# Kernel tuning notes

Hardware: AMD Instinct MI355X
Metric: run time of the kernel (lower is better)

## Reference

```python
import jax, jax.numpy as jnp
import numpy as np

N = 100000   # nodes
E = 1600000  # edges
G = 64       # graphs in batch
F_IN = 128
H = 128
SV = 64
AD = 32


def setup_inputs() -> dict:
    key = jax.random.key(0)
    ks = jax.random.split(key, 12)
    s = 0.05
    return {
        "x": jax.random.normal(ks[0], (N, F_IN), jnp.float32),
        "edge_index": jax.random.randint(ks[1], (2, E), 0, N, dtype=jnp.int64),
        "batch": jnp.sort(jax.random.randint(ks[2], (N,), 0, G, dtype=jnp.int64)),
        "state_vector": jax.random.normal(ks[3], (G, SV), jnp.float32),
        "action": jax.random.normal(ks[4], (G, AD), jnp.float32),
        "W1": jax.random.normal(ks[5], (F_IN, H), jnp.float32) * s,
        "b1": jnp.zeros((H,), jnp.float32),
        "W2": jax.random.normal(ks[6], (H, H), jnp.float32) * s,
        "b2": jnp.zeros((H,), jnp.float32),
        "Wf1": jax.random.normal(ks[7], (H + SV + AD, 256), jnp.float32) * s,
        "bf1": jnp.zeros((256,), jnp.float32),
        "Wf2": jax.random.normal(ks[8], (256, 256), jnp.float32) * s,
        "bf2": jnp.zeros((256,), jnp.float32),
        "Wo": jax.random.normal(ks[9], (256, 1), jnp.float32) * s,
        "bo": jnp.zeros((1,), jnp.float32),
    }


def gcn_conv(x, W, b, src, dst, deg_inv_sqrt):
    # PyG GCNConv: h = x @ W; aggregate D^-1/2 (A+I) D^-1/2 h; + b
    h = x @ W
    norm = deg_inv_sqrt[src] * deg_inv_sqrt[dst]          # [E]
    agg = jax.ops.segment_sum(h[src] * norm[:, None], dst, num_segments=N)
    agg = agg + h * (deg_inv_sqrt * deg_inv_sqrt)[:, None]  # self loops
    return agg + b


def reference(x, edge_index, batch, state_vector, action,
              W1, b1, W2, b2, Wf1, bf1, Wf2, bf2, Wo, bo):
    src, dst = edge_index[0], edge_index[1]
    # degree after adding self loops (aggregation index = dst, PyG default flow)
    deg = jax.ops.segment_sum(jnp.ones((E,), jnp.float32), dst, num_segments=N) + 1.0
    deg_inv_sqrt = jax.lax.rsqrt(deg)

    h = jax.nn.relu(gcn_conv(x, W1, b1, src, dst, deg_inv_sqrt))
    h = jax.nn.relu(gcn_conv(h, W2, b2, src, dst, deg_inv_sqrt))

    # global_mean_pool over graph ids
    sums = jax.ops.segment_sum(h, batch, num_segments=G)
    cnts = jax.ops.segment_sum(jnp.ones((N,), jnp.float32), batch, num_segments=G)
    pooled = sums / jnp.maximum(cnts, 1.0)[:, None]       # [G, H]

    z = jnp.concatenate([pooled, state_vector, action], axis=1)  # [G, H+SV+AD]
    z = jax.nn.relu(z @ Wf1 + bf1)
    z = jax.nn.relu(z @ Wf2 + bf2)
    return z @ Wo + bo                                     # [G, 1]
```

## Files before the change

kernel.cpp:

```cpp
#include <hip/hip_runtime.h>
#include <hip/hip_bf16.h>
#include <stdint.h>

#define N_NODES 100000
#define N_EDGES 1600000
#define N_GRAPHS 64
#define HDIM 128

#define BUCKET_SHIFT 9
#define NBUCK ((N_NODES + 511) >> 9)
#define CAP 9728
#define SCAT_CHUNK 8192
#define SCAT_NBLK ((N_EDGES + SCAT_CHUNK - 1) / SCAT_CHUNK)
#define GB_NBLK ((N_NODES + 255) / 256)

typedef __bf16 bf16x8 __attribute__((ext_vector_type(8)));
typedef float f32x4 __attribute__((ext_vector_type(4)));
typedef float f32x2 __attribute__((ext_vector_type(2)));

__global__ __launch_bounds__(256) void setup_kernel(const int* __restrict__ batch,
                                                    int* __restrict__ gstart,
                                                    const float* __restrict__ W1,
                                                    const float* __restrict__ W2,
                                                    __hip_bfloat16* __restrict__ Wt1,
                                                    __hip_bfloat16* __restrict__ Wt2,
                                                    int* __restrict__ gcur,
                                                    float* __restrict__ psum) {
    int bid = blockIdx.x;
    if (bid < GB_NBLK) {
        int i = bid * 256 + threadIdx.x;
        if (i >= N_NODES) return;
        int b = batch[i];
        int prev = (i == 0) ? -1 : batch[i - 1];
        for (int g = prev + 1; g <= b; ++g) gstart[g] = i;
        if (i == N_NODES - 1) {
            for (int g = b + 1; g <= N_GRAPHS; ++g) gstart[g] = N_NODES;
        }
    } else if (bid < GB_NBLK + 128) {
        int t = bid - GB_NBLK;
        const float* W = (t < 64) ? W1 : W2;
        __hip_bfloat16* Wt = (t < 64) ? Wt1 : Wt2;
        int bb = t & 63;
        int n = bb * 2 + (threadIdx.x >> 7);
        int k = threadIdx.x & 127;
        Wt[n * 128 + k] = __float2bfloat16(W[k * 128 + n]);
    } else {
        int i = (bid - GB_NBLK - 128) * 256 + threadIdx.x;
        if (i < NBUCK) gcur[i] = i * CAP;
        int j = i - NBUCK;
        if (j >= 0 && j < N_GRAPHS * HDIM) psum[j] = 0.f;
    }
}
#define SETUP_NBLK (GB_NBLK + 128 + (NBUCK + N_GRAPHS * HDIM + 255) / 256)

__global__ __launch_bounds__(256) void scatter_kernel(const int* __restrict__ src,
                                                      const int* __restrict__ dst,
                                                      int* __restrict__ gcur,
                                                      int* __restrict__ sorted, int E) {
    __shared__ int hist[NBUCK];
    __shared__ int base_s[NBUCK];
    int tid = threadIdx.x;
    int e0 = blockIdx.x * SCAT_CHUNK;
    int sv[SCAT_CHUNK / 256], dv[SCAT_CHUNK / 256];
#pragma unroll
    for (int j = 0; j < SCAT_CHUNK / 256; j++) {
        int e = e0 + (j << 8) + tid;
        if (e < E) { sv[j] = src[e]; dv[j] = dst[e]; } else { sv[j] = -1; dv[j] = -1; }
    }
    if (tid < NBUCK) hist[tid] = 0;
    __syncthreads();
#pragma unroll
    for (int j = 0; j < SCAT_CHUNK / 256; j++)
        if (dv[j] >= 0) atomicAdd(&hist[dv[j] >> BUCKET_SHIFT], 1);
    __syncthreads();
    if (tid < NBUCK) {
        int c = hist[tid];
        base_s[tid] = (c > 0) ? atomicAdd(&gcur[tid], c) : 0;
    }
    __syncthreads();
    if (tid < NBUCK) hist[tid] = 0;
    __syncthreads();
#pragma unroll
    for (int j = 0; j < SCAT_CHUNK / 256; j++) {
        if (dv[j] >= 0) {
            int b = dv[j] >> BUCKET_SHIFT;
            int idx = atomicAdd(&hist[b], 1);
            sorted[base_s[b] + idx] = ((dv[j] & 511) << 17) | sv[j];
        }
    }
}

__global__ __launch_bounds__(256) void bucket_build_kernel(const int* __restrict__ sorted,
                                                           const int* __restrict__ gcur,
                                                           int2* __restrict__ rs2,
                                                           float* __restrict__ dis,
                                                           int* __restrict__ csr_src) {
    __shared__ int edges[CAP];
    __shared__ int cnt[512];
    __shared__ int excl[512];
    __shared__ int ps[256];
    int b = blockIdx.x, tid = threadIdx.x;
    cnt[tid] = 0; cnt[tid + 256] = 0;
    int node0 = b << BUCKET_SHIFT;
    int lo = b * CAP, hi = gcur[b];
    int ne = hi - lo;
    for (int i = tid; i < ne; i += 256) edges[i] = sorted[lo + i];
    __syncthreads();
    for (int i = tid; i < ne; i += 256)
        atomicAdd(&cnt[((unsigned)edges[i]) >> 17], 1);
    __syncthreads();
    int c0 = cnt[2 * tid], c1 = cnt[2 * tid + 1];
    ps[tid] = c0 + c1;
    __syncthreads();
#pragma unroll
    for (int off = 1; off < 256; off <<= 1) {
        int t = (tid >= off) ? ps[tid - off] : 0;
        __syncthreads();
        ps[tid] += t;
        __syncthreads();
    }
    int pex = ps[tid] - (c0 + c1);
    excl[2 * tid] = pex;
    excl[2 * tid + 1] = pex + c0;
    __syncthreads();
#pragma unroll
    for (int k = 0; k < 2; k++) {
        int li = tid + k * 256;
        int node = node0 + li;
        if (node < N_NODES) {
            int st = lo + excl[li] + li;
            int c = cnt[li];
            rs2[node] = make_int2(st, st + c + 1);
            dis[node] = rsqrtf((float)c + 1.0f);
            csr_src[st + c] = node;
        }
    }
    cnt[tid] = 0; cnt[tid + 256] = 0;
    __syncthreads();
    for (int i = tid; i < ne; i += 256) {
        int v = edges[i];
        int li = ((unsigned)v) >> 17;
        int idx = atomicAdd(&cnt[li], 1);
        csr_src[lo + excl[li] + li + idx] = v & 0x1FFFF;
    }
}

template<bool A_FP32>
__global__ __launch_bounds__(256) void gemm_mfma_kernel(const void* __restrict__ Av,
                                                        const __hip_bfloat16* __restrict__ Wt,
                                                        const float* __restrict__ scale,
                                                        unsigned char* __restrict__ C, int nrows) {
    __shared__ float Cs[64 * 132];
    int tid = threadIdx.x;
    int wave = tid >> 6, lane = tid & 63;
    int quad = lane >> 4, l16 = lane & 15;
    int row0 = blockIdx.x * 64;
    int arow = row0 + wave * 16 + l16;
    int arow_c = min(arow, nrows - 1);

    const __hip_bfloat16* A16 = (const __hip_bfloat16*)Av;
    const float* A32 = (const float*)Av;

    f32x4 acc[8];
#pragma unroll
    for (int t = 0; t < 8; t++) acc[t] = (f32x4){0.f, 0.f, 0.f, 0.f};

#pragma unroll
    for (int kt = 0; kt < 4; kt++) {
        int kbase = kt * 32 + quad * 8;
        union { bf16x8 v; __hip_bfloat16 h[8]; uint4 u; } au;
        if (A_FP32) {
            const float* ap = A32 + (size_t)arow_c * 128 + kbase;
            float4 u0 = *(const float4*)ap;
            float4 u1 = *(const float4*)(ap + 4);
            au.h[0] = __float2bfloat16(u0.x); au.h[1] = __float2bfloat16(u0.y);
            au.h[2] = __float2bfloat16(u0.z); au.h[3] = __float2bfloat16(u0.w);
            au.h[4] = __float2bfloat16(u1.x); au.h[5] = __float2bfloat16(u1.y);
            au.h[6] = __float2bfloat16(u1.z); au.h[7] = __float2bfloat16(u1.w);
        } else {
            au.u = *(const uint4*)(A16 + (size_t)arow_c * 128 + kbase);
        }
#pragma unroll
        for (int t = 0; t < 8; t++) {
            bf16x8 b = *(const bf16x8*)(Wt + (size_t)(t * 16 + l16) * 128 + kbase);
            acc[t] = __builtin_amdgcn_mfma_f32_16x16x32_bf16(au.v, b, acc[t], 0, 0, 0);
        }
    }

    int rbase = wave * 16 + quad * 4;
    float s[4];
#pragma unroll
    for (int r = 0; r < 4; r++) s[r] = scale[min(row0 + rbase + r, nrows - 1)];
#pragma unroll
    for (int t = 0; t < 8; t++) {
#pragma unroll
        for (int r = 0; r < 4; r++)
            Cs[(rbase + r) * 132 + t * 16 + l16] = acc[t][r] * s[r];
    }
    __syncthreads();

#pragma unroll
    for (int p = 0; p < 4; p++) {
        int g = p * 256 + tid;
        int row = g >> 4, c8 = (g & 15) * 8;
        int grow = row0 + row;
        if (grow < nrows) {
            const float* cp = &Cs[row * 132 + c8];
            float4 v0 = *(const float4*)cp;
            float4 v1 = *(const float4*)(cp + 4);
            int w0 = __builtin_amdgcn_cvt_pk_fp8_f32(v0.x, v0.y, 0, false);
            w0 = __builtin_amdgcn_cvt_pk_fp8_f32(v0.z, v0.w, w0, true);
            int w1 = __builtin_amdgcn_cvt_pk_fp8_f32(v1.x, v1.y, 0, false);
            w1 = __builtin_amdgcn_cvt_pk_fp8_f32(v1.z, v1.w, w1, true);
            *(uint2*)(C + (size_t)grow * 128 + c8) = make_uint2((unsigned)w0, (unsigned)w1);
        }
    }
}

__device__ __forceinline__ void accum8p(f32x2* acc, uint2 u) {
    acc[0] += __builtin_amdgcn_cvt_pk_f32_fp8((int)u.x, false);
    acc[1] += __builtin_amdgcn_cvt_pk_f32_fp8((int)u.x, true);
    acc[2] += __builtin_amdgcn_cvt_pk_f32_fp8((int)u.y, false);
    acc[3] += __builtin_amdgcn_cvt_pk_f32_fp8((int)u.y, true);
}

__global__ __launch_bounds__(256, 8) void agg_kernel(const unsigned char* __restrict__ h8,
                                                     const float* __restrict__ dis,
                                                     const int2* __restrict__ rs2,
                                                     const int* __restrict__ csr_src,
                                                     const float* __restrict__ bias,
                                                     __hip_bfloat16* __restrict__ out, int n) {
    int wid = threadIdx.x >> 6;
    int lane = threadIdx.x & 63;
    int half = lane >> 5;
    int q = lane >> 4;
    int f = lane & 15;
    int l32 = lane & 31;
    int sub = q & 1;
    int hb = half << 5;
    unsigned fo = (unsigned)(f * 8);

    int nodeA = blockIdx.x * 8 + wid * 2;
    if (nodeA >= n) return;
    int nodeB = nodeA + 1;
    bool hasB = nodeB < n;
    int myNode = half ? (hasB ? nodeB : nodeA) : nodeA;

    int2 se = rs2[myNode];
    int i0 = se.x;
    int deg = se.y - se.x;
    if (half && !hasB) deg = 0;
    float dn = dis[myNode];

    f32x2 acc[4];
#pragma unroll
    for (int j = 0; j < 4; j++) acc[j] = (f32x2){0.f, 0.f};

    for (int base = 0; base < deg; base += 32) {
        int cnt = min(deg - base, 32);
        int idx = csr_src[i0 + base + min(l32, cnt - 1)];
        int e = 0;
        for (; e + 16 <= cnt; e += 16) {
            int s0 = __shfl(idx, hb + e + sub, 64);
            int s1 = __shfl(idx, hb + e + 2 + sub, 64);
            int s2 = __shfl(idx, hb + e + 4 + sub, 64);
            int s3 = __shfl(idx, hb + e + 6 + sub, 64);
            int s4 = __shfl(idx, hb + e + 8 + sub, 64);
            int s5 = __shfl(idx, hb + e + 10 + sub, 64);
            int s6 = __shfl(idx, hb + e + 12 + sub, 64);
            int s7 = __shfl(idx, hb + e + 14 + sub, 64);
            uint2 u0 = *(const uint2*)(h8 + (unsigned)(s0 << 7) + fo);
            uint2 u1 = *(const uint2*)(h8 + (unsigned)(s1 << 7) + fo);
            uint2 u2 = *(const uint2*)(h8 + (unsigned)(s2 << 7) + fo);
            uint2 u3 = *(const uint2*)(h8 + (unsigned)(s3 << 7) + fo);
            uint2 u4 = *(const uint2*)(h8 + (unsigned)(s4 << 7) + fo);
            uint2 u5 = *(const uint2*)(h8 + (unsigned)(s5 << 7) + fo);
            uint2 u6 = *(const uint2*)(h8 + (unsigned)(s6 << 7) + fo);
            uint2 u7 = *(const uint2*)(h8 + (unsigned)(s7 << 7) + fo);
            accum8p(acc, u0);
            accum8p(acc, u1);
            accum8p(acc, u2);
            accum8p(acc, u3);
            accum8p(acc, u4);
            accum8p(acc, u5);
            accum8p(acc, u6);
            accum8p(acc, u7);
        }
        if (e < cnt) {
            int r = cnt - 1;
#pragma unroll
            for (int k = 0; k < 8; k++) {
                int ln = e + 2 * k + sub;
                int s = __shfl(idx, hb + min(ln, r), 64);
                uint2 u = *(const uint2*)(h8 + (unsigned)(s << 7) + fo);
                if (ln > r) { u.x = 0u; u.y = 0u; }
                accum8p(acc, u);
            }
        }
    }

#pragma unroll
    for (int j = 0; j < 4; j++) {
        f32x2 v = acc[j];
        v[0] += __shfl_down(v[0], 16, 64);
        v[1] += __shfl_down(v[1], 16, 64);
        acc[j] = v;
    }

    if (sub == 0 && (half == 0 || hasB)) {
        float4 b0 = *(const float4*)(bias + f * 8);
        float4 b1 = *(const float4*)(bias + f * 8 + 4);
        float r0 = fmaxf(fmaf(acc[0][0], dn, b0.x), 0.f);
        float r1 = fmaxf(fmaf(acc[0][1], dn, b0.y), 0.f);
        float r2 = fmaxf(fmaf(acc[1][0], dn, b0.z), 0.f);
        float r3 = fmaxf(fmaf(acc[1][1], dn, b0.w), 0.f);
        float r4 = fmaxf(fmaf(acc[2][0], dn, b1.x), 0.f);
        float r5 = fmaxf(fmaf(acc[2][1], dn, b1.y), 0.f);
        float r6 = fmaxf(fmaf(acc[3][0], dn, b1.z), 0.f);
        float r7 = fmaxf(fmaf(acc[3][1], dn, b1.w), 0.f);
        __hip_bfloat162 p0 = __float22bfloat162_rn(make_float2(r0, r1));
        __hip_bfloat162 p1 = __float22bfloat162_rn(make_float2(r2, r3));
        __hip_bfloat162 p2 = __float22bfloat162_rn(make_float2(r4, r5));
        __hip_bfloat162 p3 = __float22bfloat162_rn(make_float2(r6, r7));
        uint4 pk;
        pk.x = *(unsigned int*)&p0; pk.y = *(unsigned int*)&p1;
        pk.z = *(unsigned int*)&p2; pk.w = *(unsigned int*)&p3;
        *(uint4*)(out + (size_t)myNode * 128 + f * 8) = pk;
    }
}

#define POOL_ROWS 128
__global__ __launch_bounds__(256) void pool_kernel(const __hip_bfloat16* __restrict__ h,
                                                   const int* __restrict__ batch,
                                                   const int* __restrict__ gstart,
                                                   float* __restrict__ psum, int n) {
    __shared__ float red[16 * 128];
    int tid = threadIdx.x;
    int rr = tid >> 4, fg = tid & 15;
    int r0 = blockIdx.x * POOL_ROWS;
    if (r0 >= n) return;
    int r1 = min(n, r0 + POOL_ROWS);
    int g = batch[r0];
    int seg_lo = r0;
    while (seg_lo < r1) {
        while (gstart[g + 1] <= seg_lo) g++;
        int seg_hi = min(r1, gstart[g + 1]);
        float a[8];
#pragma unroll
        for (int j = 0; j < 8; j++) a[j] = 0.f;
        for (int r = seg_lo + rr; r < seg_hi; r += 16) {
            uint4 u = *(const uint4*)(h + (size_t)r * 128 + fg * 8);
            float2 f0 = __bfloat1622float2(*(__hip_bfloat162*)&u.x);
            float2 f1 = __bfloat1622float2(*(__hip_bfloat162*)&u.y);
            float2 f2 = __bfloat1622float2(*(__hip_bfloat162*)&u.z);
            float2 f3 = __bfloat1622float2(*(__hip_bfloat162*)&u.w);
            a[0] += f0.x; a[1] += f0.y; a[2] += f1.x; a[3] += f1.y;
            a[4] += f2.x; a[5] += f2.y; a[6] += f3.x; a[7] += f3.y;
        }
        *(float4*)&red[rr * 128 + fg * 8] = make_float4(a[0], a[1], a[2], a[3]);
        *(float4*)&red[rr * 128 + fg * 8 + 4] = make_float4(a[4], a[5], a[6], a[7]);
        __syncthreads();
        if (tid < 128) {
            float s = 0.f;
#pragma unroll
            for (int k = 0; k < 16; k++) s += red[k * 128 + tid];
            atomicAdd(&psum[g * 128 + tid], s);
        }
        __syncthreads();
        seg_lo = seg_hi;
    }
}

__global__ __launch_bounds__(256) void mlp_kernel(const float* __restrict__ psum,
                                                  const int* __restrict__ gstart,
                                                  const float* __restrict__ sv,
                                                  const float* __restrict__ act,
                                                  const float* __restrict__ Wf1,
                                                  const float* __restrict__ bf1,
                                                  const float* __restrict__ Wf2,
                                                  const float* __restrict__ bf2,
                                                  const float* __restrict__ Wo,
                                                  const float* __restrict__ bo,
                                                  float* __restrict__ out) {
    int g = blockIdx.x, tid = threadIdx.x;
    __shared__ float z[224];
    __shared__ float z1[256];
    __shared__ float red[256];
    if (tid < 128) {
        int c = gstart[g + 1] - gstart[g];
        float cnt = fmaxf((float)c, 1.f);
        z[tid] = psum[g * 128 + tid] / cnt;
    } else if (tid < 192) {
        z[tid] = sv[g * 64 + (tid - 128)];
    } else if (tid < 224) {
        z[tid] = act[g * 32 + (tid - 192)];
    }
    __syncthreads();
    float a = bf1[tid];
    for (int k = 0; k < 224; k++) a = fmaf(z[k], Wf1[k * 256 + tid], a);
    z1[tid] = fmaxf(a, 0.f);
    __syncthreads();
    float b = bf2[tid];
    for (int k = 0; k < 256; k++) b = fmaf(z1[k], Wf2[k * 256 + tid], b);
    b = fmaxf(b, 0.f);
    red[tid] = b * Wo[tid];
    __syncthreads();
    for (int off = 128; off > 0; off >>= 1) {
        if (tid < off) red[tid] += red[tid + off];
        __syncthreads();
    }
    if (tid == 0) out[g] = red[0] + bo[0];
}

extern "C" void kernel_launch(void* const* d_in, const int* in_sizes, int n_in,
                              void* d_out, int out_size, void* d_ws, size_t ws_size,
                              hipStream_t stream) {
    const float* x   = (const float*)d_in[0];
    const int*   eidx = (const int*)d_in[1];
    const int*   batch = (const int*)d_in[2];
    const float* sv  = (const float*)d_in[3];
    const float* act = (const float*)d_in[4];
    const float* W1  = (const float*)d_in[5];
    const float* b1  = (const float*)d_in[6];
    const float* W2  = (const float*)d_in[7];
    const float* b2  = (const float*)d_in[8];
    const float* Wf1 = (const float*)d_in[9];
    const float* bf1 = (const float*)d_in[10];
    const float* Wf2 = (const float*)d_in[11];
    const float* bf2 = (const float*)d_in[12];
    const float* Wo  = (const float*)d_in[13];
    const float* bo  = (const float*)d_in[14];
    float* out = (float*)d_out;

    const int* srcp = eidx;
    const int* dstp = eidx + N_EDGES;

    char* w = (char*)d_ws;
    int* gcur = (int*)w;               w += (size_t)NBUCK * 4;
    float* psum = (float*)w;           w += (size_t)N_GRAPHS * HDIM * 4;
    int2* rs2 = (int2*)w;              w += (size_t)N_NODES * 8;
    float* dis = (float*)w;            w += (size_t)N_NODES * 4;
    int* gstart = (int*)w;             w += (size_t)(N_GRAPHS + 1) * 4;
    w = (char*)(((uintptr_t)w + 255) & ~(uintptr_t)255);
    int* csr_src = (int*)w;            w += (size_t)NBUCK * CAP * 4;
    w = (char*)(((uintptr_t)w + 255) & ~(uintptr_t)255);
    int* sorted = (int*)w;             w += (size_t)NBUCK * CAP * 4;
    w = (char*)(((uintptr_t)w + 255) & ~(uintptr_t)255);
    __hip_bfloat16* Wt1 = (__hip_bfloat16*)w;   w += (size_t)HDIM * HDIM * 2;
    __hip_bfloat16* Wt2 = (__hip_bfloat16*)w;   w += (size_t)HDIM * HDIM * 2;
    w = (char*)(((uintptr_t)w + 255) & ~(uintptr_t)255);
    unsigned char* hbuf = (unsigned char*)w;    w += (size_t)N_NODES * HDIM;
    w = (char*)(((uintptr_t)w + 255) & ~(uintptr_t)255);
    __hip_bfloat16* abuf = (__hip_bfloat16*)w;  w += (size_t)N_NODES * HDIM * 2;

    setup_kernel<<<SETUP_NBLK, 256, 0, stream>>>(batch, gstart, W1, W2, Wt1, Wt2, gcur, psum);

    scatter_kernel<<<SCAT_NBLK, 256, 0, stream>>>(srcp, dstp, gcur, sorted, N_EDGES);
    bucket_build_kernel<<<NBUCK, 256, 0, stream>>>(sorted, gcur, rs2, dis, csr_src);

    int gemm_blocks = (N_NODES + 63) / 64;
    int agg_blocks = (N_NODES + 7) / 8;

    gemm_mfma_kernel<true><<<gemm_blocks, 256, 0, stream>>>(x, Wt1, dis, hbuf, N_NODES);
    agg_kernel<<<agg_blocks, 256, 0, stream>>>(hbuf, dis, rs2, csr_src, b1, abuf, N_NODES);
    gemm_mfma_kernel<false><<<gemm_blocks, 256, 0, stream>>>(abuf, Wt2, dis, hbuf, N_NODES);
    agg_kernel<<<agg_blocks, 256, 0, stream>>>(hbuf, dis, rs2, csr_src, b2, abuf, N_NODES);

    pool_kernel<<<(N_NODES + POOL_ROWS - 1) / POOL_ROWS, 256, 0, stream>>>(abuf, batch, gstart, psum, N_NODES);
    mlp_kernel<<<N_GRAPHS, 256, 0, stream>>>(psum, gstart, sv, act, Wf1, bf1, Wf2, bf2, Wo, bo, out);
}
```

Measured before the change: 293.9 us.

## Fuse bucket CSR build with first GEMM via global degree counters

Counts node in-degrees with global atomics inside the scatter kernel, so the first GEMM can compute its rsqrt scale directly instead of waiting for the bucket build to produce it. The bucket build and the first GEMM are then merged into one launch with heterogeneous blocks that share a static LDS buffer. This removes one launch and lets the two independent phases overlap. In exchange it adds 1.6M global atomic increments in the scatter kernel, and the merged kernel carries the larger shared-memory footprint, which may lower occupancy for the GEMM blocks.

Result: slower. 348.7 us (+18.6%).

```diff
diff --git a/kernel.cpp b/kernel.cpp
--- a/kernel.cpp
+++ b/kernel.cpp
@@ -12,6 +12,7 @@
 #define CAP 9728
 #define SCAT_CHUNK 8192
 #define SCAT_NBLK ((N_EDGES + SCAT_CHUNK - 1) / SCAT_CHUNK)
+#define GEMM_NBLK ((N_NODES + 63) / 64)
 #define GB_NBLK ((N_NODES + 255) / 256)
 
 typedef __bf16 bf16x8 __attribute__((ext_vector_type(8)));
@@ -25,7 +26,8 @@
                                                     __hip_bfloat16* __restrict__ Wt1,
                                                     __hip_bfloat16* __restrict__ Wt2,
                                                     int* __restrict__ gcur,
-                                                    float* __restrict__ psum) {
+                                                    float* __restrict__ psum,
+                                                    int* __restrict__ deg) {
     int bid = blockIdx.x;
     if (bid < GB_NBLK) {
         int i = bid * 256 + threadIdx.x;
@@ -49,14 +51,17 @@
         if (i < NBUCK) gcur[i] = i * CAP;
         int j = i - NBUCK;
         if (j >= 0 && j < N_GRAPHS * HDIM) psum[j] = 0.f;
-    }
-}
-#define SETUP_NBLK (GB_NBLK + 128 + (NBUCK + N_GRAPHS * HDIM + 255) / 256)
+        int k = j - N_GRAPHS * HDIM;
+        if (k >= 0 && k < N_NODES) deg[k] = 0;
+    }
+}
+#define SETUP_NBLK (GB_NBLK + 128 + (NBUCK + N_GRAPHS * HDIM + N_NODES + 255) / 256)
 
 __global__ __launch_bounds__(256) void scatter_kernel(const int* __restrict__ src,
                                                       const int* __restrict__ dst,
                                                       int* __restrict__ gcur,
-                                                      int* __restrict__ sorted, int E) {
+                                                      int* __restrict__ sorted,
+                                                      int* __restrict__ deg, int E) {
     __shared__ int hist[NBUCK];
     __shared__ int base_s[NBUCK];
     int tid = threadIdx.x;
@@ -71,7 +76,10 @@
     __syncthreads();
 #pragma unroll
     for (int j = 0; j < SCAT_CHUNK / 256; j++)
-        if (dv[j] >= 0) atomicAdd(&hist[dv[j] >> BUCKET_SHIFT], 1);
+        if (dv[j] >= 0) {
+            atomicAdd(&hist[dv[j] >> BUCKET_SHIFT], 1);
+            atomicAdd(&deg[dv[j]], 1);
+        }
     __syncthreads();
     if (tid < NBUCK) {
         int c = hist[tid];
@@ -90,16 +98,16 @@
     }
 }
 
-__global__ __launch_bounds__(256) void bucket_build_kernel(const int* __restrict__ sorted,
-                                                           const int* __restrict__ gcur,
-                                                           int2* __restrict__ rs2,
-                                                           float* __restrict__ dis,
-                                                           int* __restrict__ csr_src) {
-    __shared__ int edges[CAP];
-    __shared__ int cnt[512];
-    __shared__ int excl[512];
-    __shared__ int ps[256];
-    int b = blockIdx.x, tid = threadIdx.x;
+__device__ void bucket_body(const int* __restrict__ sorted,
+                            const int* __restrict__ gcur,
+                            int2* __restrict__ rs2,
+                            float* __restrict__ dis,
+                            int* __restrict__ csr_src, int b, char* smem) {
+    int* edges = (int*)smem;
+    int* cnt = edges + CAP;
+    int* excl = cnt + 512;
+    int* ps = excl + 512;
+    int tid = threadIdx.x;
     cnt[tid] = 0; cnt[tid + 256] = 0;
     int node0 = b << BUCKET_SHIFT;
     int lo = b * CAP, hi = gcur[b];
@@ -145,16 +153,16 @@
     }
 }
 
-template<bool A_FP32>
-__global__ __launch_bounds__(256) void gemm_mfma_kernel(const void* __restrict__ Av,
-                                                        const __hip_bfloat16* __restrict__ Wt,
-                                                        const float* __restrict__ scale,
-                                                        unsigned char* __restrict__ C, int nrows) {
-    __shared__ float Cs[64 * 132];
+template<bool A_FP32, bool DEG_SCALE>
+__device__ void gemm_body(const void* __restrict__ Av,
+                          const __hip_bfloat16* __restrict__ Wt,
+                          const void* __restrict__ scp,
+                          unsigned char* __restrict__ C, int nrows, int bid,
+                          float* Cs ) {
     int tid = threadIdx.x;
     int wave = tid >> 6, lane = tid & 63;
     int quad = lane >> 4, l16 = lane & 15;
-    int row0 = blockIdx.x * 64;
+    int row0 = bid * 64;
     int arow = row0 + wave * 16 + l16;
     int arow_c = min(arow, nrows - 1);
 
@@ -190,7 +198,11 @@
     int rbase = wave * 16 + quad * 4;
     float s[4];
 #pragma unroll
-    for (int r = 0; r < 4; r++) s[r] = scale[min(row0 + rbase + r, nrows - 1)];
+    for (int r = 0; r < 4; r++) {
+        int row = min(row0 + rbase + r, nrows - 1);
+        if (DEG_SCALE) s[r] = rsqrtf((float)((const int*)scp)[row] + 1.0f);
+        else           s[r] = ((const float*)scp)[row];
+    }
 #pragma unroll
     for (int t = 0; t < 8; t++) {
 #pragma unroll
@@ -215,6 +227,31 @@
             *(uint2*)(C + (size_t)grow * 128 + c8) = make_uint2((unsigned)w0, (unsigned)w1);
         }
     }
+}
+
+__global__ __launch_bounds__(256) void build_gemm1_kernel(const int* __restrict__ sorted,
+                                                          const int* __restrict__ gcur,
+                                                          int2* __restrict__ rs2,
+                                                          float* __restrict__ dis,
+                                                          int* __restrict__ csr_src,
+                                                          const float* __restrict__ x,
+                                                          const __hip_bfloat16* __restrict__ Wt1,
+                                                          const int* __restrict__ deg,
+                                                          unsigned char* __restrict__ hbuf) {
+    __shared__ __align__(16) char smem[(CAP + 512 + 512 + 256) * 4];
+    if (blockIdx.x < NBUCK) {
+        bucket_body(sorted, gcur, rs2, dis, csr_src, blockIdx.x, smem);
+    } else {
+        gemm_body<true, true>(x, Wt1, deg, hbuf, N_NODES, blockIdx.x - NBUCK, (float*)smem);
+    }
+}
+
+__global__ __launch_bounds__(256) void gemm_mfma_kernel(const void* __restrict__ Av,
+                                                        const __hip_bfloat16* __restrict__ Wt,
+                                                        const float* __restrict__ scale,
+                                                        unsigned char* __restrict__ C, int nrows) {
+    __shared__ float Cs[64 * 132];
+    gemm_body<false, false>(Av, Wt, scale, C, nrows, blockIdx.x, Cs);
 }
 
 __device__ __forceinline__ void accum8p(f32x2* acc, uint2 u) {
@@ -440,6 +477,7 @@
     float* psum = (float*)w;           w += (size_t)N_GRAPHS * HDIM * 4;
     int2* rs2 = (int2*)w;              w += (size_t)N_NODES * 8;
     float* dis = (float*)w;            w += (size_t)N_NODES * 4;
+    int* deg = (int*)w;                w += (size_t)N_NODES * 4;
     int* gstart = (int*)w;             w += (size_t)(N_GRAPHS + 1) * 4;
     w = (char*)(((uintptr_t)w + 255) & ~(uintptr_t)255);
     int* csr_src = (int*)w;            w += (size_t)NBUCK * CAP * 4;
@@ -453,17 +491,17 @@
     w = (char*)(((uintptr_t)w + 255) & ~(uintptr_t)255);
     __hip_bfloat16* abuf = (__hip_bfloat16*)w;  w += (size_t)N_NODES * HDIM * 2;
 
-    setup_kernel<<<SETUP_NBLK, 256, 0, stream>>>(batch, gstart, W1, W2, Wt1, Wt2, gcur, psum);
-
-    scatter_kernel<<<SCAT_NBLK, 256, 0, stream>>>(srcp, dstp, gcur, sorted, N_EDGES);
-    bucket_build_kernel<<<NBUCK, 256, 0, stream>>>(sorted, gcur, rs2, dis, csr_src);
-
-    int gemm_blocks = (N_NODES + 63) / 64;
+    setup_kernel<<<SETUP_NBLK, 256, 0, stream>>>(batch, gstart, W1, W2, Wt1, Wt2, gcur, psum, deg);
+
+    scatter_kernel<<<SCAT_NBLK, 256, 0, stream>>>(srcp, dstp, gcur, sorted, deg, N_EDGES);
+
+    build_gemm1_kernel<<<NBUCK + GEMM_NBLK, 256, 0, stream>>>(sorted, gcur, rs2, dis, csr_src,
+                                                              x, Wt1, deg, hbuf);
+
     int agg_blocks = (N_NODES + 7) / 8;
 
-    gemm_mfma_kernel<true><<<gemm_blocks, 256, 0, stream>>>(x, Wt1, dis, hbuf, N_NODES);
     agg_kernel<<<agg_blocks, 256, 0, stream>>>(hbuf, dis, rs2, csr_src, b1, abuf, N_NODES);
-    gemm_mfma_kernel<false><<<gemm_blocks, 256, 0, stream>>>(abuf, Wt2, dis, hbuf, N_NODES);
+    gemm_mfma_kernel<<<GEMM_NBLK, 256, 0, stream>>>(abuf, Wt2, dis, hbuf, N_NODES);
     agg_kernel<<<agg_blocks, 256, 0, stream>>>(hbuf, dis, rs2, csr_src, b2, abuf, N_NODES);
 
     pool_kernel<<<(N_NODES + POOL_ROWS - 1) / POOL_ROWS, 256, 0, stream>>>(abuf, batch, gstart, psum, N_NODES);
```

## Fuse global mean-pool sums into second aggregation kernel epilogue

Applied to the files above, without the earlier changes.

The second GCN aggregation kernel now accumulates its ReLU outputs directly into per-graph pooled sums. It reduces within a block in shared memory when all 8 nodes of the block belong to one graph, and falls back to per-element global atomics otherwise. This removes the separate pool kernel, one launch, and the write and re-read of the bf16 activation buffer. In exchange it adds a block barrier and shared atomics to every aggregation block, and issues about 12.5k global atomic bursts into a small 64x128 psum array, which could contend.

Result: slower. 349.9 us (+19.1%).

```diff
diff --git a/kernel.cpp b/kernel.cpp
--- a/kernel.cpp
+++ b/kernel.cpp
@@ -224,14 +224,19 @@
     acc[3] += __builtin_amdgcn_cvt_pk_f32_fp8((int)u.y, true);
 }
 
+template<bool FUSE_POOL>
 __global__ __launch_bounds__(256, 8) void agg_kernel(const unsigned char* __restrict__ h8,
                                                      const float* __restrict__ dis,
                                                      const int2* __restrict__ rs2,
                                                      const int* __restrict__ csr_src,
                                                      const float* __restrict__ bias,
-                                                     __hip_bfloat16* __restrict__ out, int n) {
-    int wid = threadIdx.x >> 6;
-    int lane = threadIdx.x & 63;
+                                                     __hip_bfloat16* __restrict__ out,
+                                                     const int* __restrict__ batch,
+                                                     float* __restrict__ psum, int n) {
+    __shared__ float psum_s[128];
+    int tid = threadIdx.x;
+    int wid = tid >> 6;
+    int lane = tid & 63;
     int half = lane >> 5;
     int q = lane >> 4;
     int f = lane & 15;
@@ -239,17 +244,25 @@
     int sub = q & 1;
     int hb = half << 5;
     unsigned fo = (unsigned)(f * 8);
-
-    int nodeA = blockIdx.x * 8 + wid * 2;
-    if (nodeA >= n) return;
+    int blk0 = (int)blockIdx.x * 8;
+
+    if (FUSE_POOL) {
+        if (tid < 128) psum_s[tid] = 0.f;
+        __syncthreads();
+    }
+
+    int nodeA = blk0 + wid * 2;
+    bool active = nodeA < n;
+    if (!FUSE_POOL && !active) return;
     int nodeB = nodeA + 1;
     bool hasB = nodeB < n;
     int myNode = half ? (hasB ? nodeB : nodeA) : nodeA;
+    myNode = min(myNode, n - 1);
 
     int2 se = rs2[myNode];
     int i0 = se.x;
     int deg = se.y - se.x;
-    if (half && !hasB) deg = 0;
+    if ((half && !hasB) || !active) deg = 0;
     float dn = dis[myNode];
 
     f32x2 acc[4];
@@ -307,67 +320,60 @@
         acc[j] = v;
     }
 
-    if (sub == 0 && (half == 0 || hasB)) {
-        float4 b0 = *(const float4*)(bias + f * 8);
-        float4 b1 = *(const float4*)(bias + f * 8 + 4);
-        float r0 = fmaxf(fmaf(acc[0][0], dn, b0.x), 0.f);
-        float r1 = fmaxf(fmaf(acc[0][1], dn, b0.y), 0.f);
-        float r2 = fmaxf(fmaf(acc[1][0], dn, b0.z), 0.f);
-        float r3 = fmaxf(fmaf(acc[1][1], dn, b0.w), 0.f);
-        float r4 = fmaxf(fmaf(acc[2][0], dn, b1.x), 0.f);
-        float r5 = fmaxf(fmaf(acc[2][1], dn, b1.y), 0.f);
-        float r6 = fmaxf(fmaf(acc[3][0], dn, b1.z), 0.f);
-        float r7 = fmaxf(fmaf(acc[3][1], dn, b1.w), 0.f);
-        __hip_bfloat162 p0 = __float22bfloat162_rn(make_float2(r0, r1));
-        __hip_bfloat162 p1 = __float22bfloat162_rn(make_float2(r2, r3));
-        __hip_bfloat162 p2 = __float22bfloat162_rn(make_float2(r4, r5));
-        __hip_bfloat162 p3 = __float22bfloat162_rn(make_float2(r6, r7));
-        uint4 pk;
-        pk.x = *(unsigned int*)&p0; pk.y = *(unsigned int*)&p1;
-        pk.z = *(unsigned int*)&p2; pk.w = *(unsigned int*)&p3;
-        *(uint4*)(out + (size_t)myNode * 128 + f * 8) = pk;
-    }
-}
-
-#define POOL_ROWS 128
-__global__ __launch_bounds__(256) void pool_kernel(const __hip_bfloat16* __restrict__ h,
-                                                   const int* __restrict__ batch,
-                                                   const int* __restrict__ gstart,
-                                                   float* __restrict__ psum, int n) {
-    __shared__ float red[16 * 128];
-    int tid = threadIdx.x;
-    int rr = tid >> 4, fg = tid & 15;
-    int r0 = blockIdx.x * POOL_ROWS;
-    if (r0 >= n) return;
-    int r1 = min(n, r0 + POOL_ROWS);
-    int g = batch[r0];
-    int seg_lo = r0;
-    while (seg_lo < r1) {
-        while (gstart[g + 1] <= seg_lo) g++;
-        int seg_hi = min(r1, gstart[g + 1]);
-        float a[8];
-#pragma unroll
-        for (int j = 0; j < 8; j++) a[j] = 0.f;
-        for (int r = seg_lo + rr; r < seg_hi; r += 16) {
-            uint4 u = *(const uint4*)(h + (size_t)r * 128 + fg * 8);
-            float2 f0 = __bfloat1622float2(*(__hip_bfloat162*)&u.x);
-            float2 f1 = __bfloat1622float2(*(__hip_bfloat162*)&u.y);
-            float2 f2 = __bfloat1622float2(*(__hip_bfloat162*)&u.z);
-            float2 f3 = __bfloat1622float2(*(__hip_bfloat162*)&u.w);
-            a[0] += f0.x; a[1] += f0.y; a[2] += f1.x; a[3] += f1.y;
-            a[4] += f2.x; a[5] += f2.y; a[6] += f3.x; a[7] += f3.y;
-        }
-        *(float4*)&red[rr * 128 + fg * 8] = make_float4(a[0], a[1], a[2], a[3]);
-        *(float4*)&red[rr * 128 + fg * 8 + 4] = make_float4(a[4], a[5], a[6], a[7]);
-        __syncthreads();
-        if (tid < 128) {
-            float s = 0.f;
-#pragma unroll
-            for (int k = 0; k < 16; k++) s += red[k * 128 + tid];
-            atomicAdd(&psum[g * 128 + tid], s);
-        }
-        __syncthreads();
-        seg_lo = seg_hi;
+    bool res = active && (sub == 0) && (half == 0 || hasB);
+
+    if (FUSE_POOL) {
+        float rv[8];
+        if (res) {
+            float4 b0 = *(const float4*)(bias + f * 8);
+            float4 b1 = *(const float4*)(bias + f * 8 + 4);
+            float bb[8] = {b0.x, b0.y, b0.z, b0.w, b1.x, b1.y, b1.z, b1.w};
+#pragma unroll
+            for (int k = 0; k < 4; k++) {
+                rv[2 * k]     = fmaxf(fmaf(acc[k][0], dn, bb[2 * k]), 0.f);
+                rv[2 * k + 1] = fmaxf(fmaf(acc[k][1], dn, bb[2 * k + 1]), 0.f);
+            }
+        }
+        int gA = batch[min(blk0, n - 1)];
+        int gB = batch[min(blk0 + 7, n - 1)];
+        if (gA == gB) {
+            if (res) {
+#pragma unroll
+                for (int k = 0; k < 8; k++) atomicAdd(&psum_s[f * 8 + k], rv[k]);
+            }
+            __syncthreads();
+            if (tid < 128) {
+                float v = psum_s[tid];
+                if (v != 0.f) atomicAdd(&psum[gA * 128 + tid], v);
+            }
+        } else {
+            if (res) {
+                int g = batch[myNode];
+#pragma unroll
+                for (int k = 0; k < 8; k++) atomicAdd(&psum[g * 128 + f * 8 + k], rv[k]);
+            }
+        }
+    } else {
+        if (res) {
+            float4 b0 = *(const float4*)(bias + f * 8);
+            float4 b1 = *(const float4*)(bias + f * 8 + 4);
+            float r0 = fmaxf(fmaf(acc[0][0], dn, b0.x), 0.f);
+            float r1 = fmaxf(fmaf(acc[0][1], dn, b0.y), 0.f);
+            float r2 = fmaxf(fmaf(acc[1][0], dn, b0.z), 0.f);
+            float r3 = fmaxf(fmaf(acc[1][1], dn, b0.w), 0.f);
+            float r4 = fmaxf(fmaf(acc[2][0], dn, b1.x), 0.f);
+            float r5 = fmaxf(fmaf(acc[2][1], dn, b1.y), 0.f);
+            float r6 = fmaxf(fmaf(acc[3][0], dn, b1.z), 0.f);
+            float r7 = fmaxf(fmaf(acc[3][1], dn, b1.w), 0.f);
+            __hip_bfloat162 p0 = __float22bfloat162_rn(make_float2(r0, r1));
+            __hip_bfloat162 p1 = __float22bfloat162_rn(make_float2(r2, r3));
+            __hip_bfloat162 p2 = __float22bfloat162_rn(make_float2(r4, r5));
+            __hip_bfloat162 p3 = __float22bfloat162_rn(make_float2(r6, r7));
+            uint4 pk;
+            pk.x = *(unsigned int*)&p0; pk.y = *(unsigned int*)&p1;
+            pk.z = *(unsigned int*)&p2; pk.w = *(unsigned int*)&p3;
+            *(uint4*)(out + (size_t)myNode * 128 + f * 8) = pk;
+        }
     }
 }
 
@@ -462,10 +468,11 @@
     int agg_blocks = (N_NODES + 7) / 8;
 
     gemm_mfma_kernel<true><<<gemm_blocks, 256, 0, stream>>>(x, Wt1, dis, hbuf, N_NODES);
-    agg_kernel<<<agg_blocks, 256, 0, stream>>>(hbuf, dis, rs2, csr_src, b1, abuf, N_NODES);
+    agg_kernel<false><<<agg_blocks, 256, 0, stream>>>(hbuf, dis, rs2, csr_src, b1, abuf,
+                                                      batch, psum, N_NODES);
     gemm_mfma_kernel<false><<<gemm_blocks, 256, 0, stream>>>(abuf, Wt2, dis, hbuf, N_NODES);
-    agg_kernel<<<agg_blocks, 256, 0, stream>>>(hbuf, dis, rs2, csr_src, b2, abuf, N_NODES);
-
-    pool_kernel<<<(N_NODES + POOL_ROWS - 1) / POOL_ROWS, 256, 0, stream>>>(abuf, batch, gstart, psum, N_NODES);
+    agg_kernel<true><<<agg_blocks, 256, 0, stream>>>(hbuf, dis, rs2, csr_src, b2, abuf,
+                                                     batch, psum, N_NODES);
+
     mlp_kernel<<<N_GRAPHS, 256, 0, stream>>>(psum, gstart, sv, act, Wf1, bf1, Wf2, bf2, Wo, bo, out);
 }
```
